# Performance work log

Hardware: AMD Instinct MI355X
Metric: run time of the kernel (lower is better)

Reference implementation:

```python
import jax, jax.numpy as jnp
import numpy as np

N_NODES = 100000
N_EDGES = 1000000
F_IN = 64
F_HID = 64
F_OUT = 2
NUM_GRAPHS = 64


def setup_inputs() -> dict:
    key = jax.random.key(0)
    ks = jax.random.split(key, 8)
    x = jax.random.normal(ks[0], (N_NODES, F_IN), dtype=jnp.float32)
    edge_index = jax.random.randint(ks[1], (2, N_EDGES), 0, N_NODES, dtype=jnp.int32)
    batch = jnp.sort(jax.random.randint(ks[2], (N_NODES,), 0, NUM_GRAPHS, dtype=jnp.int32))
    s1 = 1.0 / np.sqrt(F_IN)
    s2 = 1.0 / np.sqrt(F_HID)
    W1 = jax.random.normal(ks[3], (F_IN, F_HID), dtype=jnp.float32) * s1
    W2 = jax.random.normal(ks[4], (F_HID, F_HID), dtype=jnp.float32) * s2
    W3 = jax.random.normal(ks[5], (F_HID, F_HID), dtype=jnp.float32) * s2
    Wlin = jax.random.normal(ks[6], (F_HID, F_OUT), dtype=jnp.float32) * s2
    return {
        "x": x, "edge_index": edge_index, "batch": batch,
        "W1": W1, "b1": jnp.zeros((F_HID,), jnp.float32),
        "W2": W2, "b2": jnp.zeros((F_HID,), jnp.float32),
        "W3": W3, "b3": jnp.zeros((F_HID,), jnp.float32),
        "Wlin": Wlin, "blin": jnp.zeros((F_OUT,), jnp.float32),
    }


def _gcn_norm(edge_index, n_nodes):
    # add self-loops, compute symmetric D^-1/2 (A+I) D^-1/2 edge weights
    loops = jnp.arange(n_nodes, dtype=edge_index.dtype)
    src = jnp.concatenate([edge_index[0], loops])  # message source j
    dst = jnp.concatenate([edge_index[1], loops])  # aggregation target i
    deg = jax.ops.segment_sum(jnp.ones_like(dst, dtype=jnp.float32), dst,
                              num_segments=n_nodes)
    dinv = jnp.where(deg > 0, jax.lax.rsqrt(deg), 0.0)
    norm = dinv[src] * dinv[dst]  # [E+N]
    return src, dst, norm


def _gcn_conv(h, W, b, src, dst, norm, n_nodes):
    h = h @ W                                    # [N, F] dense transform first (PyG order)
    msg = h[src] * norm[:, None]                 # gather + scale  [E+N, F]
    agg = jax.ops.segment_sum(msg, dst, num_segments=n_nodes)
    return agg + b


def reference(x, edge_index, batch, W1, b1, W2, b2, W3, b3, Wlin, blin):
    n = x.shape[0]
    src, dst, norm = _gcn_norm(edge_index, n)
    h = jax.nn.relu(_gcn_conv(x, W1, b1, src, dst, norm, n))
    h = jax.nn.relu(_gcn_conv(h, W2, b2, src, dst, norm, n))
    h = _gcn_conv(h, W3, b3, src, dst, norm, n)
    # global mean pool over graphs
    sums = jax.ops.segment_sum(h, batch, num_segments=NUM_GRAPHS)        # [G, F]
    cnts = jax.ops.segment_sum(jnp.ones((n,), jnp.float32), batch,
                               num_segments=NUM_GRAPHS)
    pooled = sums / jnp.maximum(cnts, 1.0)[:, None]
    # dropout(p=0.1) is identity in eval mode
    return pooled @ Wlin + blin
```

## Files before the change

### kernel.cpp

```cpp
#include <hip/hip_runtime.h>

#define FDIM 64

typedef unsigned short u16;
typedef unsigned int u32;
typedef float v2f __attribute__((ext_vector_type(2)));

__device__ __forceinline__ u16 f2bf(float x) {
    unsigned int u = __float_as_uint(x);
    return (u16)((u + 0x7fff + ((u >> 16) & 1)) >> 16);
}
__device__ __forceinline__ float bf2f(u16 h) {
    return __uint_as_float(((unsigned int)h) << 16);
}
__device__ __forceinline__ u32 pk_fp8x4(float a, float b, float c, float d) {
    u32 p = __builtin_amdgcn_cvt_pk_fp8_f32(a, b, 0, false);
    p = __builtin_amdgcn_cvt_pk_fp8_f32(c, d, p, true);
    return p;
}


template <bool BF16IN>
__device__ __forceinline__ void mm_tile64(
    const void* __restrict__ ain, const float* __restrict__ bias, int do_relu,
    u32* __restrict__ t, int n, int blk,
    float (*__restrict__ As)[FDIM + 1], float* __restrict__ Ws)
{
    int tid = threadIdx.x;
    int r0 = blk * 64;

    #pragma unroll
    for (int i = 0; i < 4; ++i) {
        int idx = tid + 256 * i;
        int r = idx >> 4;
        int kq = idx & 15;
        float4 v = make_float4(0.f, 0.f, 0.f, 0.f);
        int R = r0 + r;
        if (R < n) {
            if (BF16IN) {
                ushort4 h = ((const ushort4*)ain)[(size_t)R * 16 + kq];
                v.x = bf2f(h.x); v.y = bf2f(h.y); v.z = bf2f(h.z); v.w = bf2f(h.w);
            } else {
                v = ((const float4*)ain)[(size_t)R * 16 + kq];
            }
            if (bias != nullptr) {
                float4 b = ((const float4*)bias)[kq];
                v.x += b.x; v.y += b.y; v.z += b.z; v.w += b.w;
            }
            if (do_relu) {
                v.x = fmaxf(v.x, 0.f); v.y = fmaxf(v.y, 0.f);
                v.z = fmaxf(v.z, 0.f); v.w = fmaxf(v.w, 0.f);
            }
        }
        As[r][kq * 4 + 0] = v.x;
        As[r][kq * 4 + 1] = v.y;
        As[r][kq * 4 + 2] = v.z;
        As[r][kq * 4 + 3] = v.w;
    }
    __syncthreads();

    int rq = tid >> 4;
    int cq = tid & 15;
    float acc[4][4];
    #pragma unroll
    for (int i = 0; i < 4; ++i)
        #pragma unroll
        for (int j = 0; j < 4; ++j) acc[i][j] = 0.f;

    const float4* Ws4 = (const float4*)Ws;
    #pragma unroll 4
    for (int k = 0; k < FDIM; ++k) {
        float4 w = Ws4[k * 16 + cq];
        float a[4];
        #pragma unroll
        for (int i = 0; i < 4; ++i) a[i] = As[rq * 4 + i][k];
        #pragma unroll
        for (int i = 0; i < 4; ++i) {
            acc[i][0] = fmaf(a[i], w.x, acc[i][0]);
            acc[i][1] = fmaf(a[i], w.y, acc[i][1]);
            acc[i][2] = fmaf(a[i], w.z, acc[i][2]);
            acc[i][3] = fmaf(a[i], w.w, acc[i][3]);
        }
    }

    #pragma unroll
    for (int i = 0; i < 4; ++i) {
        int R = r0 + rq * 4 + i;
        if (R < n)
            t[(size_t)R * 16 + cq] =
                pk_fp8x4(acc[i][0], acc[i][1], acc[i][2], acc[i][3]);
    }
}

__global__ __launch_bounds__(256) void k_matmul_h(
    const u16* __restrict__ ain, const float* __restrict__ Wm,
    const float* __restrict__ bias, u32* __restrict__ t, int n)
{
    __shared__ float As[64][FDIM + 1];
    __shared__ float Ws[FDIM * FDIM];
    int tid = threadIdx.x;
    #pragma unroll
    for (int i = 0; i < 4; ++i)
        ((float4*)Ws)[tid + 256 * i] = ((const float4*)Wm)[tid + 256 * i];
    mm_tile64<true>(ain, bias, 1, t, n, blockIdx.x, As, Ws);
}


__global__ __launch_bounds__(256) void k_mm_fill(
    const float* __restrict__ x, const float* __restrict__ W1,
    u32* __restrict__ t,
    const int* __restrict__ src, const int* __restrict__ dst,
    int* __restrict__ cnt, int* __restrict__ csr,
    int n, int E, int cap, int fill_blocks)
{
    __shared__ float As[64][FDIM + 1];
    __shared__ float Ws[FDIM * FDIM];

    if ((int)blockIdx.x < fill_blocks) {
        int stride = fill_blocks * 256;
        int e = blockIdx.x * 256 + threadIdx.x;
        for (; e + 7 * stride < E; e += 8 * stride) {
            int d[8], s[8], p[8];
            #pragma unroll
            for (int u = 0; u < 8; ++u)
                d[u] = __builtin_nontemporal_load(&dst[e + u * stride]);
            #pragma unroll
            for (int u = 0; u < 8; ++u)
                s[u] = __builtin_nontemporal_load(&src[e + u * stride]);
            #pragma unroll
            for (int u = 0; u < 8; ++u) p[u] = atomicAdd(&cnt[d[u]], 1);
            #pragma unroll
            for (int u = 0; u < 8; ++u)
                if (p[u] < cap) csr[(size_t)d[u] * cap + p[u]] = s[u];
        }
        for (; e < E; e += stride) {
            int d = dst[e];
            int p = atomicAdd(&cnt[d], 1);
            if (p < cap) csr[(size_t)d * cap + p] = src[e];
        }
        return;
    }

    int blk = blockIdx.x - fill_blocks;
    int tid = threadIdx.x;
    #pragma unroll
    for (int i = 0; i < 4; ++i)
        ((float4*)Ws)[tid + 256 * i] = ((const float4*)W1)[tid + 256 * i];
    mm_tile64<false>(x, nullptr, 0, t, n, blk, As, Ws);
}


__device__ __forceinline__ float4 agg_node(
    int i, const int* __restrict__ cnt, const int* __restrict__ csr,
    const u32* __restrict__ t, int cap, int li, int nbase)
{
    int deg = cnt[i];
    float di = rsqrtf((float)deg + 1.0f);
    int m = deg < cap ? deg : cap;

    u32 sp = t[(size_t)i * 16 + li];
    v2f s0 = __builtin_amdgcn_cvt_pk_f32_fp8(sp, false);
    v2f s1 = __builtin_amdgcn_cvt_pk_f32_fp8(sp, true);
    float4 A0 = make_float4(s0.x * di, s0.y * di, s1.x * di, s1.y * di);
    float4 A1 = make_float4(0.f, 0.f, 0.f, 0.f);
    float4 A2 = make_float4(0.f, 0.f, 0.f, 0.f);
    float4 A3 = make_float4(0.f, 0.f, 0.f, 0.f);

    const int* row = csr + (size_t)i * cap;

    for (int c0 = 0; c0 < m; c0 += 16) {
        int cm = m - c0; if (cm > 16) cm = 16;
        int sv = 0; float dvv = 0.f;
        if (li < cm) {
            sv = __builtin_nontemporal_load(&row[c0 + li]);
            dvv = rsqrtf((float)cnt[sv] + 1.0f);
        }
        int jv[16]; float dj[16]; u32 v[16];
        #pragma unroll
        for (int u = 0; u < 16; ++u) {
            jv[u] = __shfl(sv, nbase + u);
            dj[u] = __shfl(dvv, nbase + u);
        }
        #pragma unroll
        for (int u = 0; u < 16; ++u) v[u] = t[(size_t)jv[u] * 16 + li];
        #pragma unroll
        for (int u = 0; u < 16; ++u) {
            v2f x0 = __builtin_amdgcn_cvt_pk_f32_fp8(v[u], false);
            v2f x1 = __builtin_amdgcn_cvt_pk_f32_fp8(v[u], true);
            float4* Ap = (u & 3) == 0 ? &A0 : (u & 3) == 1 ? &A1 :
                         (u & 3) == 2 ? &A2 : &A3;
            Ap->x = fmaf(x0.x, dj[u], Ap->x);
            Ap->y = fmaf(x0.y, dj[u], Ap->y);
            Ap->z = fmaf(x1.x, dj[u], Ap->z);
            Ap->w = fmaf(x1.y, dj[u], Ap->w);
        }
    }

    float4 O;
    O.x = ((A0.x + A1.x) + (A2.x + A3.x)) * di;
    O.y = ((A0.y + A1.y) + (A2.y + A3.y)) * di;
    O.z = ((A0.z + A1.z) + (A2.z + A3.z)) * di;
    O.w = ((A0.w + A1.w) + (A2.w + A3.w)) * di;
    return O;
}


__global__ __launch_bounds__(256) void k_aggregate(
    const int* __restrict__ cnt, const int* __restrict__ csr,
    const u32* __restrict__ t, uint2* __restrict__ aggh, int n, int cap)
{
    int tid = threadIdx.x;
    long long gw = ((long long)blockIdx.x * 256 + tid) >> 6;
    int lane = tid & 63;
    int sub = lane >> 4;
    int li  = lane & 15;
    long long il = gw * 4 + sub;
    if (il >= n) return;
    int i = (int)il;

    float4 O = agg_node(i, cnt, csr, t, cap, li, sub << 4);
    uint2 pk;
    pk.x = ((u32)f2bf(O.x)) | (((u32)f2bf(O.y)) << 16);
    pk.y = ((u32)f2bf(O.z)) | (((u32)f2bf(O.w)) << 16);
    aggh[(size_t)i * 16 + li] = pk;
}


__global__ __launch_bounds__(256) void k_agg_pool(
    const int* __restrict__ cnt, const int* __restrict__ csr,
    const u32* __restrict__ t, const int* __restrict__ batch,
    float* __restrict__ partial, int n, int cap, int npart)
{
    int g = blockIdx.x / npart;
    int part = blockIdx.x - g * npart;
    int tid = threadIdx.x;

    int lo = 0, hi = n;
    while (lo < hi) { int mid = (lo + hi) >> 1; if (batch[mid] < g) lo = mid + 1; else hi = mid; }
    int start = lo;
    hi = n;
    while (lo < hi) { int mid = (lo + hi) >> 1; if (batch[mid] <= g) lo = mid + 1; else hi = mid; }
    int end = lo;

    int group = tid >> 4;
    int li = tid & 15;
    int lane = tid & 63;
    int nbase = (lane >> 4) << 4;

    float4 acc = make_float4(0.f, 0.f, 0.f, 0.f);
    for (int i = start + part * 16 + group; i < end; i += npart * 16) {
        float4 O = agg_node(i, cnt, csr, t, cap, li, nbase);
        acc.x += O.x; acc.y += O.y; acc.z += O.z; acc.w += O.w;
    }

    __shared__ float4 red[16][16];
    red[group][li] = acc;
    __syncthreads();
    if (tid < 16) {
        float4 s = make_float4(0.f, 0.f, 0.f, 0.f);
        #pragma unroll
        for (int q = 0; q < 16; ++q) {
            s.x += red[q][tid].x; s.y += red[q][tid].y;
            s.z += red[q][tid].z; s.w += red[q][tid].w;
        }
        ((float4*)partial)[((size_t)g * npart + part) * 16 + tid] = s;
    }
}

__global__ __launch_bounds__(64) void k_pool2(
    const float* __restrict__ partial, const int* __restrict__ batch,
    const float* __restrict__ b3, const float* __restrict__ Wlin,
    const float* __restrict__ blin, float* __restrict__ out,
    int n, int fout, int npart)
{
    int g = blockIdx.x;
    int tid = threadIdx.x;

    int lo = 0, hi = n;
    while (lo < hi) { int mid = (lo + hi) >> 1; if (batch[mid] < g) lo = mid + 1; else hi = mid; }
    int start = lo;
    hi = n;
    while (lo < hi) { int mid = (lo + hi) >> 1; if (batch[mid] <= g) lo = mid + 1; else hi = mid; }
    int cnt = lo - start;

    __shared__ float pooled[64];
    float v = 0.f;
    for (int p = 0; p < npart; ++p)
        v += partial[((size_t)g * npart + p) * 64 + tid];
    pooled[tid] = (cnt > 0) ? (v / (float)cnt + b3[tid]) : 0.f;
    __syncthreads();
    if (tid < fout) {
        float o = blin[tid];
        for (int k = 0; k < 64; ++k) o += pooled[k] * Wlin[k * fout + tid];
        out[(size_t)g * fout + tid] = o;
    }
}


extern "C" void kernel_launch(void* const* d_in, const int* in_sizes, int n_in,
                              void* d_out, int out_size, void* d_ws, size_t ws_size,
                              hipStream_t stream) {
    const float* x     = (const float*)d_in[0];
    const int*   ei    = (const int*)d_in[1];
    const int*   batch = (const int*)d_in[2];
    const float* W1 = (const float*)d_in[3];
    const float* b1 = (const float*)d_in[4];
    const float* W2 = (const float*)d_in[5];
    const float* b2 = (const float*)d_in[6];
    const float* W3 = (const float*)d_in[7];
    const float* b3 = (const float*)d_in[8];
    const float* Wl = (const float*)d_in[9];
    const float* bl = (const float*)d_in[10];

    int n = in_sizes[0] / 64;
    int E = in_sizes[1] / 2;
    int fout = in_sizes[10];
    int ngraphs = out_size / fout;

    const int* srcp = ei;
    const int* dstp = ei + E;

    const int npart = 16;

    float* ws   = (float*)d_ws;
    u32*   agg  = (u32*)ws;
    u32*   t    = agg + (size_t)n * 32;
    float* partial = (float*)(t + (size_t)n * 16);
    int* cnt    = (int*)(partial + 64 * npart * 64);
    int* csr    = cnt + n;

    size_t fixed = (size_t)n * 32 * 4 + (size_t)n * 16 * 4 +
                   64 * npart * 64 * 4 + (size_t)n * 4;
    int cap = 64;
    while (cap > 32 && fixed + (size_t)n * cap * 4 > ws_size) cap -= 8;

    int nb_ag = (int)((((long long)(n + 3) / 4) * 64 + 255) / 256);
    int mm_blocks = (n + 63) / 64;
    int fill_blocks = 256;

    hipMemsetAsync(cnt, 0, (size_t)n * sizeof(int), stream);
    k_mm_fill<<<fill_blocks + mm_blocks, 256, 0, stream>>>(
        x, W1, t, srcp, dstp, cnt, csr, n, E, cap, fill_blocks);

    k_aggregate<<<nb_ag, 256, 0, stream>>>(cnt, csr, t, (uint2*)agg, n, cap);
    k_matmul_h<<<mm_blocks, 256, 0, stream>>>((const u16*)agg, W2, b1, t, n);
    k_aggregate<<<nb_ag, 256, 0, stream>>>(cnt, csr, t, (uint2*)agg, n, cap);
    k_matmul_h<<<mm_blocks, 256, 0, stream>>>((const u16*)agg, W3, b2, t, n);
    k_agg_pool<<<ngraphs * npart, 256, 0, stream>>>(cnt, csr, t, batch,
                                                    partial, n, cap, npart);
    k_pool2<<<ngraphs, 64, 0, stream>>>(partial, batch, b3, Wl, bl,
                                        (float*)d_out, n, fout, npart);
}
```

Measured before the change: 269.7 us.

## Prescale features by source degree norm in matmul; interleave fill and matmul blocks

Layers 2 and 3 now multiply each matmul output row by the source node's rsqrt(deg+1) before the fp8 store, so aggregation skips the per-neighbour cnt gather and rsqrt and does plain adds. Inactive lanes index a zeroed padding row at index n instead of being masked. The first fused kernel interleaves CSR-fill blocks among matmul blocks (every third block), scales the fill block count with the node count, and halves the unroll. This removes a dependent random load per edge, at the cost of applying the scale before fp8 quantisation.

```diff
diff --git a/kernel.cpp b/kernel.cpp
--- a/kernel.cpp
+++ b/kernel.cpp
@@ -20,10 +20,10 @@
 }
 
 
-template <bool BF16IN>
+template <bool BF16IN, bool SCALE>
 __device__ __forceinline__ void mm_tile64(
     const void* __restrict__ ain, const float* __restrict__ bias, int do_relu,
-    u32* __restrict__ t, int n, int blk,
+    u32* __restrict__ t, const int* __restrict__ cnt, int n, int blk,
     float (*__restrict__ As)[FDIM + 1], float* __restrict__ Ws)
 {
     int tid = threadIdx.x;
@@ -86,15 +86,20 @@
     #pragma unroll
     for (int i = 0; i < 4; ++i) {
         int R = r0 + rq * 4 + i;
-        if (R < n)
+        if (R < n) {
+            float sc = 1.0f;
+            if (SCALE) sc = rsqrtf((float)cnt[R] + 1.0f);
             t[(size_t)R * 16 + cq] =
-                pk_fp8x4(acc[i][0], acc[i][1], acc[i][2], acc[i][3]);
+                pk_fp8x4(acc[i][0] * sc, acc[i][1] * sc,
+                         acc[i][2] * sc, acc[i][3] * sc);
+        }
     }
 }
 
 __global__ __launch_bounds__(256) void k_matmul_h(
     const u16* __restrict__ ain, const float* __restrict__ Wm,
-    const float* __restrict__ bias, u32* __restrict__ t, int n)
+    const float* __restrict__ bias, u32* __restrict__ t,
+    const int* __restrict__ cnt, int n)
 {
     __shared__ float As[64][FDIM + 1];
     __shared__ float Ws[FDIM * FDIM];
@@ -102,7 +107,7 @@
     #pragma unroll
     for (int i = 0; i < 4; ++i)
         ((float4*)Ws)[tid + 256 * i] = ((const float4*)Wm)[tid + 256 * i];
-    mm_tile64<true>(ain, bias, 1, t, n, blockIdx.x, As, Ws);
+    mm_tile64<true, true>(ain, bias, 1, t, cnt, n, blockIdx.x, As, Ws);
 }
 
 
@@ -116,21 +121,26 @@
     __shared__ float As[64][FDIM + 1];
     __shared__ float Ws[FDIM * FDIM];
 
-    if ((int)blockIdx.x < fill_blocks) {
+    int b = blockIdx.x;
+    int fb3 = fill_blocks * 3;
+    bool fill_role = (b < fb3) && ((b % 3) == 2);
+
+    if (fill_role) {
+        int fidx = b / 3;
         int stride = fill_blocks * 256;
-        int e = blockIdx.x * 256 + threadIdx.x;
-        for (; e + 7 * stride < E; e += 8 * stride) {
-            int d[8], s[8], p[8];
+        int e = fidx * 256 + threadIdx.x;
+        for (; e + 3 * stride < E; e += 4 * stride) {
+            int d[4], s[4], p[4];
             #pragma unroll
-            for (int u = 0; u < 8; ++u)
+            for (int u = 0; u < 4; ++u)
                 d[u] = __builtin_nontemporal_load(&dst[e + u * stride]);
             #pragma unroll
-            for (int u = 0; u < 8; ++u)
+            for (int u = 0; u < 4; ++u)
                 s[u] = __builtin_nontemporal_load(&src[e + u * stride]);
             #pragma unroll
-            for (int u = 0; u < 8; ++u) p[u] = atomicAdd(&cnt[d[u]], 1);
+            for (int u = 0; u < 4; ++u) p[u] = atomicAdd(&cnt[d[u]], 1);
             #pragma unroll
-            for (int u = 0; u < 8; ++u)
+            for (int u = 0; u < 4; ++u)
                 if (p[u] < cap) csr[(size_t)d[u] * cap + p[u]] = s[u];
         }
         for (; e < E; e += stride) {
@@ -141,18 +151,19 @@
         return;
     }
 
-    int blk = blockIdx.x - fill_blocks;
+    int blk = (b < fb3) ? (b - (b + 1) / 3) : (b - fill_blocks);
     int tid = threadIdx.x;
     #pragma unroll
     for (int i = 0; i < 4; ++i)
         ((float4*)Ws)[tid + 256 * i] = ((const float4*)W1)[tid + 256 * i];
-    mm_tile64<false>(x, nullptr, 0, t, n, blk, As, Ws);
-}
-
-
+    mm_tile64<false, false>(x, nullptr, 0, t, nullptr, n, blk, As, Ws);
+}
+
+
+template <bool SCALED>
 __device__ __forceinline__ float4 agg_node(
     int i, const int* __restrict__ cnt, const int* __restrict__ csr,
-    const u32* __restrict__ t, int cap, int li, int nbase)
+    const u32* __restrict__ t, int cap, int li, int nbase, int n)
 {
     int deg = cnt[i];
     float di = rsqrtf((float)deg + 1.0f);
@@ -161,25 +172,35 @@
     u32 sp = t[(size_t)i * 16 + li];
     v2f s0 = __builtin_amdgcn_cvt_pk_f32_fp8(sp, false);
     v2f s1 = __builtin_amdgcn_cvt_pk_f32_fp8(sp, true);
-    float4 A0 = make_float4(s0.x * di, s0.y * di, s1.x * di, s1.y * di);
-    float4 A1 = make_float4(0.f, 0.f, 0.f, 0.f);
-    float4 A2 = make_float4(0.f, 0.f, 0.f, 0.f);
-    float4 A3 = make_float4(0.f, 0.f, 0.f, 0.f);
+    float4 A0, A1, A2, A3;
+    if (SCALED) {
+        A0 = make_float4(s0.x, s0.y, s1.x, s1.y);
+    } else {
+        A0 = make_float4(s0.x * di, s0.y * di, s1.x * di, s1.y * di);
+    }
+    A1 = make_float4(0.f, 0.f, 0.f, 0.f);
+    A2 = make_float4(0.f, 0.f, 0.f, 0.f);
+    A3 = make_float4(0.f, 0.f, 0.f, 0.f);
 
     const int* row = csr + (size_t)i * cap;
 
     for (int c0 = 0; c0 < m; c0 += 16) {
         int cm = m - c0; if (cm > 16) cm = 16;
-        int sv = 0; float dvv = 0.f;
-        if (li < cm) {
-            sv = __builtin_nontemporal_load(&row[c0 + li]);
-            dvv = rsqrtf((float)cnt[sv] + 1.0f);
+        int sv; float dvv = 0.f;
+        if (SCALED) {
+            sv = (li < cm) ? __builtin_nontemporal_load(&row[c0 + li]) : n;
+        } else {
+            sv = 0;
+            if (li < cm) {
+                sv = __builtin_nontemporal_load(&row[c0 + li]);
+                dvv = rsqrtf((float)cnt[sv] + 1.0f);
+            }
         }
         int jv[16]; float dj[16]; u32 v[16];
         #pragma unroll
         for (int u = 0; u < 16; ++u) {
             jv[u] = __shfl(sv, nbase + u);
-            dj[u] = __shfl(dvv, nbase + u);
+            if (!SCALED) dj[u] = __shfl(dvv, nbase + u);
         }
         #pragma unroll
         for (int u = 0; u < 16; ++u) v[u] = t[(size_t)jv[u] * 16 + li];
@@ -189,10 +210,15 @@
             v2f x1 = __builtin_amdgcn_cvt_pk_f32_fp8(v[u], true);
             float4* Ap = (u & 3) == 0 ? &A0 : (u & 3) == 1 ? &A1 :
                          (u & 3) == 2 ? &A2 : &A3;
-            Ap->x = fmaf(x0.x, dj[u], Ap->x);
-            Ap->y = fmaf(x0.y, dj[u], Ap->y);
-            Ap->z = fmaf(x1.x, dj[u], Ap->z);
-            Ap->w = fmaf(x1.y, dj[u], Ap->w);
+            if (SCALED) {
+                Ap->x += x0.x; Ap->y += x0.y;
+                Ap->z += x1.x; Ap->w += x1.y;
+            } else {
+                Ap->x = fmaf(x0.x, dj[u], Ap->x);
+                Ap->y = fmaf(x0.y, dj[u], Ap->y);
+                Ap->z = fmaf(x1.x, dj[u], Ap->z);
+                Ap->w = fmaf(x1.y, dj[u], Ap->w);
+            }
         }
     }
 
@@ -205,6 +231,7 @@
 }
 
 
+template <bool SCALED>
 __global__ __launch_bounds__(256) void k_aggregate(
     const int* __restrict__ cnt, const int* __restrict__ csr,
     const u32* __restrict__ t, uint2* __restrict__ aggh, int n, int cap)
@@ -218,7 +245,7 @@
     if (il >= n) return;
     int i = (int)il;
 
-    float4 O = agg_node(i, cnt, csr, t, cap, li, sub << 4);
+    float4 O = agg_node<SCALED>(i, cnt, csr, t, cap, li, sub << 4, n);
     uint2 pk;
     pk.x = ((u32)f2bf(O.x)) | (((u32)f2bf(O.y)) << 16);
     pk.y = ((u32)f2bf(O.z)) | (((u32)f2bf(O.w)) << 16);
@@ -249,7 +276,7 @@
 
     float4 acc = make_float4(0.f, 0.f, 0.f, 0.f);
     for (int i = start + part * 16 + group; i < end; i += npart * 16) {
-        float4 O = agg_node(i, cnt, csr, t, cap, li, nbase);
+        float4 O = agg_node<true>(i, cnt, csr, t, cap, li, nbase, n);
         acc.x += O.x; acc.y += O.y; acc.z += O.z; acc.w += O.w;
     }
 
@@ -325,27 +352,29 @@
     float* ws   = (float*)d_ws;
     u32*   agg  = (u32*)ws;
     u32*   t    = agg + (size_t)n * 32;
-    float* partial = (float*)(t + (size_t)n * 16);
+    float* partial = (float*)(t + (size_t)(n + 1) * 16);
     int* cnt    = (int*)(partial + 64 * npart * 64);
     int* csr    = cnt + n;
 
-    size_t fixed = (size_t)n * 32 * 4 + (size_t)n * 16 * 4 +
+    size_t fixed = (size_t)n * 32 * 4 + (size_t)(n + 1) * 16 * 4 +
                    64 * npart * 64 * 4 + (size_t)n * 4;
     int cap = 64;
     while (cap > 32 && fixed + (size_t)n * cap * 4 > ws_size) cap -= 8;
 
     int nb_ag = (int)((((long long)(n + 3) / 4) * 64 + 255) / 256);
     int mm_blocks = (n + 63) / 64;
-    int fill_blocks = 256;
+    int fill_blocks = mm_blocks / 2;
+    int total_blocks = mm_blocks + fill_blocks;
 
     hipMemsetAsync(cnt, 0, (size_t)n * sizeof(int), stream);
-    k_mm_fill<<<fill_blocks + mm_blocks, 256, 0, stream>>>(
+    hipMemsetAsync(t + (size_t)n * 16, 0, 64, stream);
+    k_mm_fill<<<total_blocks, 256, 0, stream>>>(
         x, W1, t, srcp, dstp, cnt, csr, n, E, cap, fill_blocks);
 
-    k_aggregate<<<nb_ag, 256, 0, stream>>>(cnt, csr, t, (uint2*)agg, n, cap);
-    k_matmul_h<<<mm_blocks, 256, 0, stream>>>((const u16*)agg, W2, b1, t, n);
-    k_aggregate<<<nb_ag, 256, 0, stream>>>(cnt, csr, t, (uint2*)agg, n, cap);
-    k_matmul_h<<<mm_blocks, 256, 0, stream>>>((const u16*)agg, W3, b2, t, n);
+    k_aggregate<false><<<nb_ag, 256, 0, stream>>>(cnt, csr, t, (uint2*)agg, n, cap);
+    k_matmul_h<<<mm_blocks, 256, 0, stream>>>((const u16*)agg, W2, b1, t, cnt, n);
+    k_aggregate<true><<<nb_ag, 256, 0, stream>>>(cnt, csr, t, (uint2*)agg, n, cap);
+    k_matmul_h<<<mm_blocks, 256, 0, stream>>>((const u16*)agg, W3, b2, t, cnt, n);
     k_agg_pool<<<ngraphs * npart, 256, 0, stream>>>(cnt, csr, t, batch,
                                                     partial, n, cap, npart);
     k_pool2<<<ngraphs, 64, 0, stream>>>(partial, batch, b3, Wl, bl,
```

Result: no change. 270.0 us (+0.1%).

## Fuse aggregation with next-layer matmul and pre-scale features by source degree

Applied to the files above, without the earlier changes.

Merges each aggregate kernel with the following dense transform, so the aggregated row goes through shared memory and is never written to or read back from global memory as bf16. The matmul output is pre-multiplied by the source node's D^-1/2 before fp8 packing, which removes the per-neighbor cnt lookup, rsqrt and FMA from the next aggregation. The final pooling kernel is folded into agg_pool with a last-block-done atomic counter. The trade-offs are that each fused block serialises four gather rounds before its matmul, which may lower occupancy and parallelism, and that fp8 quantisation now happens after the degree scaling.

```diff
diff --git a/kernel.cpp b/kernel.cpp
--- a/kernel.cpp
+++ b/kernel.cpp
@@ -6,13 +6,6 @@
 typedef unsigned int u32;
 typedef float v2f __attribute__((ext_vector_type(2)));
 
-__device__ __forceinline__ u16 f2bf(float x) {
-    unsigned int u = __float_as_uint(x);
-    return (u16)((u + 0x7fff + ((u >> 16) & 1)) >> 16);
-}
-__device__ __forceinline__ float bf2f(u16 h) {
-    return __uint_as_float(((unsigned int)h) << 16);
-}
 __device__ __forceinline__ u32 pk_fp8x4(float a, float b, float c, float d) {
     u32 p = __builtin_amdgcn_cvt_pk_fp8_f32(a, b, 0, false);
     p = __builtin_amdgcn_cvt_pk_fp8_f32(c, d, p, true);
@@ -20,45 +13,12 @@
 }
 
 
-template <bool BF16IN>
-__device__ __forceinline__ void mm_tile64(
-    const void* __restrict__ ain, const float* __restrict__ bias, int do_relu,
-    u32* __restrict__ t, int n, int blk,
-    float (*__restrict__ As)[FDIM + 1], float* __restrict__ Ws)
+template <bool SCALE>
+__device__ __forceinline__ void mm_compute(
+    u32* __restrict__ t, const int* __restrict__ cnt, int n, int r0,
+    float (*__restrict__ As)[FDIM + 1], const float* __restrict__ Ws)
 {
     int tid = threadIdx.x;
-    int r0 = blk * 64;
-
-    #pragma unroll
-    for (int i = 0; i < 4; ++i) {
-        int idx = tid + 256 * i;
-        int r = idx >> 4;
-        int kq = idx & 15;
-        float4 v = make_float4(0.f, 0.f, 0.f, 0.f);
-        int R = r0 + r;
-        if (R < n) {
-            if (BF16IN) {
-                ushort4 h = ((const ushort4*)ain)[(size_t)R * 16 + kq];
-                v.x = bf2f(h.x); v.y = bf2f(h.y); v.z = bf2f(h.z); v.w = bf2f(h.w);
-            } else {
-                v = ((const float4*)ain)[(size_t)R * 16 + kq];
-            }
-            if (bias != nullptr) {
-                float4 b = ((const float4*)bias)[kq];
-                v.x += b.x; v.y += b.y; v.z += b.z; v.w += b.w;
-            }
-            if (do_relu) {
-                v.x = fmaxf(v.x, 0.f); v.y = fmaxf(v.y, 0.f);
-                v.z = fmaxf(v.z, 0.f); v.w = fmaxf(v.w, 0.f);
-            }
-        }
-        As[r][kq * 4 + 0] = v.x;
-        As[r][kq * 4 + 1] = v.y;
-        As[r][kq * 4 + 2] = v.z;
-        As[r][kq * 4 + 3] = v.w;
-    }
-    __syncthreads();
-
     int rq = tid >> 4;
     int cq = tid & 15;
     float acc[4][4];
@@ -86,23 +46,14 @@
     #pragma unroll
     for (int i = 0; i < 4; ++i) {
         int R = r0 + rq * 4 + i;
-        if (R < n)
+        if (R < n) {
+            float sc = 1.0f;
+            if (SCALE) sc = rsqrtf((float)cnt[R] + 1.0f);
             t[(size_t)R * 16 + cq] =
-                pk_fp8x4(acc[i][0], acc[i][1], acc[i][2], acc[i][3]);
-    }
-}
-
-__global__ __launch_bounds__(256) void k_matmul_h(
-    const u16* __restrict__ ain, const float* __restrict__ Wm,
-    const float* __restrict__ bias, u32* __restrict__ t, int n)
-{
-    __shared__ float As[64][FDIM + 1];
-    __shared__ float Ws[FDIM * FDIM];
-    int tid = threadIdx.x;
-    #pragma unroll
-    for (int i = 0; i < 4; ++i)
-        ((float4*)Ws)[tid + 256 * i] = ((const float4*)Wm)[tid + 256 * i];
-    mm_tile64<true>(ain, bias, 1, t, n, blockIdx.x, As, Ws);
+                pk_fp8x4(acc[i][0] * sc, acc[i][1] * sc,
+                         acc[i][2] * sc, acc[i][3] * sc);
+        }
+    }
 }
 
 
@@ -142,29 +93,51 @@
     }
 
     int blk = blockIdx.x - fill_blocks;
+    int r0 = blk * 64;
     int tid = threadIdx.x;
     #pragma unroll
     for (int i = 0; i < 4; ++i)
         ((float4*)Ws)[tid + 256 * i] = ((const float4*)W1)[tid + 256 * i];
-    mm_tile64<false>(x, nullptr, 0, t, n, blk, As, Ws);
-}
-
-
+
+    #pragma unroll
+    for (int i = 0; i < 4; ++i) {
+        int idx = tid + 256 * i;
+        int r = idx >> 4;
+        int kq = idx & 15;
+        float4 v = make_float4(0.f, 0.f, 0.f, 0.f);
+        int R = r0 + r;
+        if (R < n) v = ((const float4*)x)[(size_t)R * 16 + kq];
+        As[r][kq * 4 + 0] = v.x;
+        As[r][kq * 4 + 1] = v.y;
+        As[r][kq * 4 + 2] = v.z;
+        As[r][kq * 4 + 3] = v.w;
+    }
+    __syncthreads();
+    mm_compute<false>(t, nullptr, n, r0, As, Ws);
+}
+
+
+template <bool SCALED>
 __device__ __forceinline__ float4 agg_node(
     int i, const int* __restrict__ cnt, const int* __restrict__ csr,
     const u32* __restrict__ t, int cap, int li, int nbase)
 {
-    int deg = cnt[i];
-    float di = rsqrtf((float)deg + 1.0f);
-    int m = deg < cap ? deg : cap;
+    int dg = cnt[i];
+    float di = rsqrtf((float)dg + 1.0f);
+    int m = dg < cap ? dg : cap;
 
     u32 sp = t[(size_t)i * 16 + li];
     v2f s0 = __builtin_amdgcn_cvt_pk_f32_fp8(sp, false);
     v2f s1 = __builtin_amdgcn_cvt_pk_f32_fp8(sp, true);
-    float4 A0 = make_float4(s0.x * di, s0.y * di, s1.x * di, s1.y * di);
-    float4 A1 = make_float4(0.f, 0.f, 0.f, 0.f);
-    float4 A2 = make_float4(0.f, 0.f, 0.f, 0.f);
-    float4 A3 = make_float4(0.f, 0.f, 0.f, 0.f);
+    float4 A0, A1, A2, A3;
+    if (SCALED) {
+        A0 = make_float4(s0.x, s0.y, s1.x, s1.y);
+    } else {
+        A0 = make_float4(s0.x * di, s0.y * di, s1.x * di, s1.y * di);
+    }
+    A1 = make_float4(0.f, 0.f, 0.f, 0.f);
+    A2 = make_float4(0.f, 0.f, 0.f, 0.f);
+    A3 = make_float4(0.f, 0.f, 0.f, 0.f);
 
     const int* row = csr + (size_t)i * cap;
 
@@ -173,26 +146,34 @@
         int sv = 0; float dvv = 0.f;
         if (li < cm) {
             sv = __builtin_nontemporal_load(&row[c0 + li]);
-            dvv = rsqrtf((float)cnt[sv] + 1.0f);
+            if (!SCALED) dvv = rsqrtf((float)cnt[sv] + 1.0f);
         }
         int jv[16]; float dj[16]; u32 v[16];
         #pragma unroll
         for (int u = 0; u < 16; ++u) {
             jv[u] = __shfl(sv, nbase + u);
-            dj[u] = __shfl(dvv, nbase + u);
-        }
-        #pragma unroll
-        for (int u = 0; u < 16; ++u) v[u] = t[(size_t)jv[u] * 16 + li];
+            if (!SCALED) dj[u] = __shfl(dvv, nbase + u);
+        }
+        #pragma unroll
+        for (int u = 0; u < 16; ++u) {
+            v[u] = 0;
+            if (u < cm) v[u] = t[(size_t)jv[u] * 16 + li];
+        }
         #pragma unroll
         for (int u = 0; u < 16; ++u) {
             v2f x0 = __builtin_amdgcn_cvt_pk_f32_fp8(v[u], false);
             v2f x1 = __builtin_amdgcn_cvt_pk_f32_fp8(v[u], true);
             float4* Ap = (u & 3) == 0 ? &A0 : (u & 3) == 1 ? &A1 :
                          (u & 3) == 2 ? &A2 : &A3;
-            Ap->x = fmaf(x0.x, dj[u], Ap->x);
-            Ap->y = fmaf(x0.y, dj[u], Ap->y);
-            Ap->z = fmaf(x1.x, dj[u], Ap->z);
-            Ap->w = fmaf(x1.y, dj[u], Ap->w);
+            if (SCALED) {
+                Ap->x += x0.x; Ap->y += x0.y;
+                Ap->z += x1.x; Ap->w += x1.y;
+            } else {
+                Ap->x = fmaf(x0.x, dj[u], Ap->x);
+                Ap->y = fmaf(x0.y, dj[u], Ap->y);
+                Ap->z = fmaf(x1.x, dj[u], Ap->z);
+                Ap->w = fmaf(x1.y, dj[u], Ap->w);
+            }
         }
     }
 
@@ -205,31 +186,55 @@
 }
 
 
-__global__ __launch_bounds__(256) void k_aggregate(
+template <bool SCALED_IN>
+__global__ __launch_bounds__(256) void k_aggmm(
     const int* __restrict__ cnt, const int* __restrict__ csr,
-    const u32* __restrict__ t, uint2* __restrict__ aggh, int n, int cap)
-{
+    const u32* __restrict__ tin, const float* __restrict__ Wm,
+    const float* __restrict__ bias, u32* __restrict__ tout,
+    int n, int cap)
+{
+    __shared__ float As[64][FDIM + 1];
+    __shared__ float Ws[FDIM * FDIM];
     int tid = threadIdx.x;
-    long long gw = ((long long)blockIdx.x * 256 + tid) >> 6;
-    int lane = tid & 63;
-    int sub = lane >> 4;
-    int li  = lane & 15;
-    long long il = gw * 4 + sub;
-    if (il >= n) return;
-    int i = (int)il;
-
-    float4 O = agg_node(i, cnt, csr, t, cap, li, sub << 4);
-    uint2 pk;
-    pk.x = ((u32)f2bf(O.x)) | (((u32)f2bf(O.y)) << 16);
-    pk.y = ((u32)f2bf(O.z)) | (((u32)f2bf(O.w)) << 16);
-    aggh[(size_t)i * 16 + li] = pk;
+    #pragma unroll
+    for (int i = 0; i < 4; ++i)
+        ((float4*)Ws)[tid + 256 * i] = ((const float4*)Wm)[tid + 256 * i];
+
+    int r0 = blockIdx.x * 64;
+    int group = tid >> 4;
+    int li = tid & 15;
+    int nbase = ((tid & 63) >> 4) << 4;
+    float4 b = ((const float4*)bias)[li];
+
+    #pragma unroll 1
+    for (int r = 0; r < 4; ++r) {
+        int row = r * 16 + group;
+        int i = r0 + row;
+        float4 v = make_float4(0.f, 0.f, 0.f, 0.f);
+        if (i < n) {
+            float4 O = agg_node<SCALED_IN>(i, cnt, csr, tin, cap, li, nbase);
+            v.x = fmaxf(O.x + b.x, 0.f);
+            v.y = fmaxf(O.y + b.y, 0.f);
+            v.z = fmaxf(O.z + b.z, 0.f);
+            v.w = fmaxf(O.w + b.w, 0.f);
+        }
+        As[row][li * 4 + 0] = v.x;
+        As[row][li * 4 + 1] = v.y;
+        As[row][li * 4 + 2] = v.z;
+        As[row][li * 4 + 3] = v.w;
+    }
+    __syncthreads();
+    mm_compute<true>(tout, cnt, n, r0, As, Ws);
 }
 
 
 __global__ __launch_bounds__(256) void k_agg_pool(
     const int* __restrict__ cnt, const int* __restrict__ csr,
     const u32* __restrict__ t, const int* __restrict__ batch,
-    float* __restrict__ partial, int n, int cap, int npart)
+    float* __restrict__ partial, int* __restrict__ done,
+    const float* __restrict__ b3, const float* __restrict__ Wlin,
+    const float* __restrict__ blin, float* __restrict__ out,
+    int n, int cap, int npart, int fout)
 {
     int g = blockIdx.x / npart;
     int part = blockIdx.x - g * npart;
@@ -244,12 +249,11 @@
 
     int group = tid >> 4;
     int li = tid & 15;
-    int lane = tid & 63;
-    int nbase = (lane >> 4) << 4;
+    int nbase = ((tid & 63) >> 4) << 4;
 
     float4 acc = make_float4(0.f, 0.f, 0.f, 0.f);
     for (int i = start + part * 16 + group; i < end; i += npart * 16) {
-        float4 O = agg_node(i, cnt, csr, t, cap, li, nbase);
+        float4 O = agg_node<true>(i, cnt, csr, t, cap, li, nbase);
         acc.x += O.x; acc.y += O.y; acc.z += O.z; acc.w += O.w;
     }
 
@@ -265,29 +269,26 @@
         }
         ((float4*)partial)[((size_t)g * npart + part) * 16 + tid] = s;
     }
-}
-
-__global__ __launch_bounds__(64) void k_pool2(
-    const float* __restrict__ partial, const int* __restrict__ batch,
-    const float* __restrict__ b3, const float* __restrict__ Wlin,
-    const float* __restrict__ blin, float* __restrict__ out,
-    int n, int fout, int npart)
-{
-    int g = blockIdx.x;
-    int tid = threadIdx.x;
-
-    int lo = 0, hi = n;
-    while (lo < hi) { int mid = (lo + hi) >> 1; if (batch[mid] < g) lo = mid + 1; else hi = mid; }
-    int start = lo;
-    hi = n;
-    while (lo < hi) { int mid = (lo + hi) >> 1; if (batch[mid] <= g) lo = mid + 1; else hi = mid; }
-    int cnt = lo - start;
-
+
+    __threadfence();
+    __syncthreads();
+    __shared__ int lastflag;
+    if (tid == 0) {
+        int old = atomicAdd(&done[g], 1);
+        lastflag = (old == npart - 1);
+    }
+    __syncthreads();
+    if (!lastflag) return;
+    __threadfence();
+
+    int cg = end - start;
     __shared__ float pooled[64];
-    float v = 0.f;
-    for (int p = 0; p < npart; ++p)
-        v += partial[((size_t)g * npart + p) * 64 + tid];
-    pooled[tid] = (cnt > 0) ? (v / (float)cnt + b3[tid]) : 0.f;
+    if (tid < 64) {
+        float v = 0.f;
+        for (int p = 0; p < npart; ++p)
+            v += partial[((size_t)g * npart + p) * 64 + tid];
+        pooled[tid] = (cg > 0) ? (v / (float)cg + b3[tid]) : 0.f;
+    }
     __syncthreads();
     if (tid < fout) {
         float o = blin[tid];
@@ -322,32 +323,28 @@
 
     const int npart = 16;
 
-    float* ws   = (float*)d_ws;
-    u32*   agg  = (u32*)ws;
-    u32*   t    = agg + (size_t)n * 32;
-    float* partial = (float*)(t + (size_t)n * 16);
-    int* cnt    = (int*)(partial + 64 * npart * 64);
-    int* csr    = cnt + n;
-
-    size_t fixed = (size_t)n * 32 * 4 + (size_t)n * 16 * 4 +
-                   64 * npart * 64 * 4 + (size_t)n * 4;
+    u32* tA = (u32*)d_ws;
+    u32* tB = tA + (size_t)n * 16;
+    int* cnt = (int*)(tB + (size_t)n * 16);
+    int* done = cnt + n;
+    float* partial = (float*)(done + ngraphs);
+    int* csr = (int*)(partial + (size_t)ngraphs * npart * 64);
+
+    size_t fixed = (size_t)n * 16 * 4 * 2 + (size_t)n * 4 + (size_t)ngraphs * 4 +
+                   (size_t)ngraphs * npart * 64 * 4;
     int cap = 64;
     while (cap > 32 && fixed + (size_t)n * cap * 4 > ws_size) cap -= 8;
 
-    int nb_ag = (int)((((long long)(n + 3) / 4) * 64 + 255) / 256);
     int mm_blocks = (n + 63) / 64;
     int fill_blocks = 256;
 
-    hipMemsetAsync(cnt, 0, (size_t)n * sizeof(int), stream);
+    hipMemsetAsync(cnt, 0, (size_t)(n + ngraphs) * sizeof(int), stream);
     k_mm_fill<<<fill_blocks + mm_blocks, 256, 0, stream>>>(
-        x, W1, t, srcp, dstp, cnt, csr, n, E, cap, fill_blocks);
-
-    k_aggregate<<<nb_ag, 256, 0, stream>>>(cnt, csr, t, (uint2*)agg, n, cap);
-    k_matmul_h<<<mm_blocks, 256, 0, stream>>>((const u16*)agg, W2, b1, t, n);
-    k_aggregate<<<nb_ag, 256, 0, stream>>>(cnt, csr, t, (uint2*)agg, n, cap);
-    k_matmul_h<<<mm_blocks, 256, 0, stream>>>((const u16*)agg, W3, b2, t, n);
-    k_agg_pool<<<ngraphs * npart, 256, 0, stream>>>(cnt, csr, t, batch,
-                                                    partial, n, cap, npart);
-    k_pool2<<<ngraphs, 64, 0, stream>>>(partial, batch, b3, Wl, bl,
-                                        (float*)d_out, n, fout, npart);
-}
+        x, W1, tA, srcp, dstp, cnt, csr, n, E, cap, fill_blocks);
+
+    k_aggmm<false><<<mm_blocks, 256, 0, stream>>>(cnt, csr, tA, W2, b1, tB, n, cap);
+    k_aggmm<true><<<mm_blocks, 256, 0, stream>>>(cnt, csr, tB, W3, b2, tA, n, cap);
+    k_agg_pool<<<ngraphs * npart, 256, 0, stream>>>(
+        cnt, csr, tA, batch, partial, done, b3, Wl, bl,
+        (float*)d_out, n, cap, npart, fout);
+}
```

Measured after the change: 354.4 us. +31.4%, slower.
